# Kernel tuning notes

Measured on AMD Instinct MI355X. Metric: run time of the kernel, lower is better.

Reference implementation:

```python
import jax, jax.numpy as jnp
import numpy as np

B, L, H, D = 1, 2048, 24, 128
HID = H * D            # 3072
MLP = 4 * HID          # 12288
EPS = 1e-6


def setup_inputs() -> dict:
    key = jax.random.key(0)
    ks = jax.random.split(key, 8)
    w = lambda k, shape: jax.random.normal(k, shape, jnp.float32) * 0.02
    return {
        "x": jax.random.normal(ks[0], (B, L, HID), jnp.float32),
        "vec": jax.random.normal(ks[1], (B, HID), jnp.float32),
        "pe": jax.random.normal(ks[2], (1, 1, L, D // 2, 2, 2), jnp.float32),
        # Modulation(double=False): Dense(3*hidden)
        "mod_w": w(ks[3], (HID, 3 * HID)),
        "mod_b": jnp.zeros((3 * HID,), jnp.float32),
        # pre_norm LayerNormalization (gamma/beta)
        "ln_gamma": jnp.ones((HID,), jnp.float32),
        "ln_beta": jnp.zeros((HID,), jnp.float32),
        # linear1: Dense(3*hidden + mlp_hidden)
        "w1": w(ks[4], (HID, 3 * HID + MLP)),
        "b1": jnp.zeros((3 * HID + MLP,), jnp.float32),
        # QKNorm scales (per head_dim)
        "q_scale": jnp.ones((D,), jnp.float32),
        "k_scale": jnp.ones((D,), jnp.float32),
        # linear2: Dense(hidden), input hidden + mlp_hidden
        "w2": w(ks[5], (HID + MLP, HID)),
        "b2": jnp.zeros((HID,), jnp.float32),
    }


def _rmsnorm(t, scale):
    # RMSNorm over last (head) dim, eps=1e-6
    return t * jax.lax.rsqrt(jnp.mean(jnp.square(t), axis=-1, keepdims=True) + EPS) * scale


def _apply_rope(t, pe):
    # t: (B,H,L,D) -> view (B,H,L,D/2,1,2); pe: (1,1,L,D/2,2,2)
    t_ = t.reshape(*t.shape[:-1], -1, 1, 2)
    out = pe[..., 0] * t_[..., 0] + pe[..., 1] * t_[..., 1]  # (B,H,L,D/2,2)
    return out.reshape(t.shape)


def reference(x, vec, pe, mod_w, mod_b, ln_gamma, ln_beta, w1, b1,
              q_scale, k_scale, w2, b2):
    # Modulation: silu -> Dense -> split into shift/scale/gate, each [B,1,HID]
    mod = (jax.nn.silu(vec) @ mod_w + mod_b)[:, None, :]
    shift, scale, gate = jnp.split(mod, 3, axis=-1)

    # pre_norm LayerNorm (eps=1e-6) + modulation affine
    mu = jnp.mean(x, axis=-1, keepdims=True)
    var = jnp.mean(jnp.square(x - mu), axis=-1, keepdims=True)
    ln = (x - mu) * jax.lax.rsqrt(var + EPS) * ln_gamma + ln_beta
    x_mod = (1.0 + scale) * ln + shift

    # linear1 -> split qkv / mlp branches
    h = x_mod @ w1 + b1
    qkv, mlp = h[..., : 3 * HID], h[..., 3 * HID:]

    # 'B L (K H D) -> K B H L D'
    qkv = qkv.reshape(B, L, 3, H, D).transpose(2, 0, 3, 1, 4)
    q, k, v = qkv[0], qkv[1], qkv[2]

    # QK RMSNorm + RoPE
    q = _apply_rope(_rmsnorm(q, q_scale), pe)
    k = _apply_rope(_rmsnorm(k, k_scale), pe)

    # scaled dot-product attention
    scores = jnp.einsum("bhqd,bhkd->bhqk", q, k) * (D ** -0.5)
    attn = jnp.einsum("bhqk,bhkd->bhqd", jax.nn.softmax(scores, axis=-1), v)
    attn = attn.transpose(0, 2, 1, 3).reshape(B, L, HID)  # B H L D -> B L (H D)

    # concat attention + gelu(mlp, tanh approx) -> linear2, gated residual
    out = jnp.concatenate([attn, jax.nn.gelu(mlp, approximate=True)], axis=-1) @ w2 + b2
    return x + gate * out
```

## Files before the change

### kernel.cpp

```cpp
#include <hip/hip_runtime.h>
#include <hip/hip_bf16.h>
#include <cstdint>

#define L_SEQ 2048
#define NH    24
#define DH    128
#define HID   3072
#define MLPD  12288
#define N1    21504
#define K2    15360
#define EPSF  1e-6f
#define ATT_SCALE 0.08838834764831845f

typedef __bf16 bf16x8 __attribute__((ext_vector_type(8)));
typedef float  f32x4  __attribute__((ext_vector_type(4)));

__device__ __forceinline__ float gelu_tanh(float x) {
    float x3 = x * x * x;
    return 0.5f * x * (1.f + tanhf(0.7978845608028654f * (x + 0.044715f * x3)));
}

__device__ __forceinline__ unsigned short f2bf(float f) {
    union { float f; unsigned int u; } x{f};
    unsigned int r = x.u + 0x7fffu + ((x.u >> 16) & 1u);
    return (unsigned short)(r >> 16);
}

__device__ __forceinline__ void gload_lds16(const void* g, void* l) {
    __builtin_amdgcn_global_load_lds(
        (__attribute__((address_space(1))) void*)g,
        (__attribute__((address_space(3))) void*)l, 16, 0, 0);
}

__global__ __launch_bounds__(256)
void k_convT(const float* __restrict__ in, unsigned short* __restrict__ out,
             int R, int C) {
    __shared__ unsigned short s[64][72];
    const int r0 = blockIdx.y * 64, c0 = blockIdx.x * 64;
    const int tid = threadIdx.x;
    const int row = tid >> 4, c4 = (tid & 15) * 4;
    #pragma unroll
    for (int rr = 0; rr < 4; rr++) {
        int r = row + rr * 16;
        float4 v = *(const float4*)&in[(size_t)(r0 + r) * C + c0 + c4];
        s[r][c4 + 0] = f2bf(v.x); s[r][c4 + 1] = f2bf(v.y);
        s[r][c4 + 2] = f2bf(v.z); s[r][c4 + 3] = f2bf(v.w);
    }
    __syncthreads();
    #pragma unroll
    for (int rr = 0; rr < 4; rr++) {
        int oc = row + rr * 16;
        ushort4 t = make_ushort4(s[c4 + 0][oc], s[c4 + 1][oc],
                                 s[c4 + 2][oc], s[c4 + 3][oc]);
        *(ushort4*)&out[(size_t)(c0 + oc) * R + r0 + c4] = t;
    }
}

__global__ __launch_bounds__(256)
void k_mod(const float* __restrict__ vec, const float* __restrict__ mod_w,
           const float* __restrict__ mod_b, float* __restrict__ mod) {
    __shared__ float sv[384];
    const int j  = blockIdx.x * 256 + threadIdx.x;
    const int k0 = blockIdx.y * 384;
    for (int i = threadIdx.x; i < 384; i += 256) {
        float v = vec[k0 + i];
        sv[i] = v / (1.f + __expf(-v));
    }
    __syncthreads();
    float acc = (blockIdx.y == 0) ? mod_b[j] : 0.f;
    #pragma unroll 8
    for (int i = 0; i < 384; i++)
        acc = fmaf(sv[i], mod_w[(size_t)(k0 + i) * 9216 + j], acc);
    atomicAdd(&mod[j], acc);
}

__global__ __launch_bounds__(256)
void k_ln(const float* __restrict__ x, const float* __restrict__ mod,
          const float* __restrict__ gamma, const float* __restrict__ beta,
          unsigned short* __restrict__ x_mod) {
    __shared__ float rs_[4], rs2_[4];
    const int l = blockIdx.x, tid = threadIdx.x;
    const float* xr = x + (size_t)l * HID;
    float s = 0.f, s2 = 0.f;
    for (int i = tid; i < HID; i += 256) {
        float v = xr[i]; s += v; s2 = fmaf(v, v, s2);
    }
    #pragma unroll
    for (int off = 32; off; off >>= 1) { s += __shfl_xor(s, off); s2 += __shfl_xor(s2, off); }
    const int w = tid >> 6;
    if ((tid & 63) == 0) { rs_[w] = s; rs2_[w] = s2; }
    __syncthreads();
    s  = rs_[0] + rs_[1] + rs_[2] + rs_[3];
    s2 = rs2_[0] + rs2_[1] + rs2_[2] + rs2_[3];
    float mu   = s * (1.f / HID);
    float var  = s2 * (1.f / HID) - mu * mu;
    float rstd = rsqrtf(var + EPSF);
    unsigned short* orow = x_mod + (size_t)l * HID;
    for (int i = tid; i < HID; i += 256) {
        float ln = (xr[i] - mu) * rstd * gamma[i] + beta[i];
        orow[i] = f2bf(fmaf(1.f + mod[HID + i], ln, mod[i]));
    }
}

template<int MODE>
__global__ __launch_bounds__(256)
void gemm_bt(const unsigned short* __restrict__ A,
             const unsigned short* __restrict__ Bt,
             const float* __restrict__ bias, int K,
             float* __restrict__ qkv, unsigned short* __restrict__ vt,
             unsigned short* __restrict__ a2,
             const float* __restrict__ xres, const float* __restrict__ mod,
             float* __restrict__ out) {
    __shared__ unsigned short As[128 * 32];
    __shared__ unsigned short Bs[128 * 32];
    const int tid = threadIdx.x;
    const int bm = blockIdx.y * 128, bn = blockIdx.x * 128;
    const int w = tid >> 6, lane = tid & 63;
    const int wm = w >> 1, wn = w & 1;
    const int quad = lane >> 4, lr = lane & 15;
    const int srow = lane >> 2, spart = lane & 3;

    f32x4 acc[4][4] = {};

    for (int k0 = 0; k0 < K; k0 += 32) {
        #pragma unroll
        for (int s = 0; s < 2; s++) {
            const int slot = w + s * 4;
            gload_lds16(&A [(size_t)(bm + slot * 16 + srow) * K + k0 + spart * 8],
                        &As[slot * 512]);
            gload_lds16(&Bt[(size_t)(bn + slot * 16 + srow) * K + k0 + spart * 8],
                        &Bs[slot * 512]);
        }
        __syncthreads();
        bf16x8 af[4], bfr[4];
        #pragma unroll
        for (int t = 0; t < 4; t++) {
            af[t]  = *(const bf16x8*)&As[(wm * 64 + t * 16 + lr) * 32 + quad * 8];
            bfr[t] = *(const bf16x8*)&Bs[(wn * 64 + t * 16 + lr) * 32 + quad * 8];
        }
        #pragma unroll
        for (int mt = 0; mt < 4; mt++)
            #pragma unroll
            for (int nt = 0; nt < 4; nt++)
                acc[mt][nt] = __builtin_amdgcn_mfma_f32_16x16x32_bf16(
                    af[mt], bfr[nt], acc[mt][nt], 0, 0, 0);
        __syncthreads();
    }

    #pragma unroll
    for (int mt = 0; mt < 4; mt++) {
        #pragma unroll
        for (int nt = 0; nt < 4; nt++) {
            const int col = bn + wn * 64 + nt * 16 + lr;
            const float bs = bias[col];
            #pragma unroll
            for (int r = 0; r < 4; r++) {
                const int row = bm + wm * 64 + mt * 16 + quad * 4 + r;
                float v = acc[mt][nt][r] + bs;
                if (MODE == 0) {
                    if (col < 2 * HID) {
                        int s3 = col / HID, rem = col - s3 * HID;
                        int hh = rem >> 7, d = rem & 127;
                        qkv[(((size_t)s3 * NH + hh) * L_SEQ + row) * DH + d] = v;
                    } else if (col < 3 * HID) {
                        int rem = col - 2 * HID;
                        int hh = rem >> 7, d = rem & 127;
                        vt[((size_t)hh * DH + d) * L_SEQ + row] = f2bf(v);
                    } else {
                        a2[(size_t)row * K2 + col - 6144] = f2bf(gelu_tanh(v));
                    }
                } else {
                    out[(size_t)row * HID + col] =
                        fmaf(mod[2 * HID + col], v, xres[(size_t)row * HID + col]);
                }
            }
        }
    }
}

__global__ __launch_bounds__(64)
void k_rmsrope(const float* __restrict__ qkv, const float* __restrict__ pe,
               const float* __restrict__ qsc, const float* __restrict__ ksc,
               unsigned short* __restrict__ qb, unsigned short* __restrict__ kb) {
    const int idx = blockIdx.x;
    const int h = idx >> 11, l = idx & 2047;
    const int p = threadIdx.x;
    const float* qp = qkv + ((size_t)h * L_SEQ + l) * DH;
    const float* kp = qkv + ((size_t)(NH + h) * L_SEQ + l) * DH;
    const float4 pv = *(const float4*)&pe[((size_t)l * 64 + p) * 4];
    const float2 qs2 = *(const float2*)&qsc[2 * p];
    const float2 ks2 = *(const float2*)&ksc[2 * p];

    float2 t = *(const float2*)&qp[2 * p];
    float ss = fmaf(t.x, t.x, t.y * t.y);
    #pragma unroll
    for (int off = 32; off; off >>= 1) ss += __shfl_xor(ss, off);
    float r = rsqrtf(ss * (1.f / DH) + EPSF);
    float a = t.x * r * qs2.x, b = t.y * r * qs2.y;
    *(ushort2*)&qb[((size_t)h * L_SEQ + l) * DH + 2 * p] =
        make_ushort2(f2bf(fmaf(pv.x, a, pv.y * b) * ATT_SCALE),
                     f2bf(fmaf(pv.z, a, pv.w * b) * ATT_SCALE));

    t = *(const float2*)&kp[2 * p];
    ss = fmaf(t.x, t.x, t.y * t.y);
    #pragma unroll
    for (int off = 32; off; off >>= 1) ss += __shfl_xor(ss, off);
    r = rsqrtf(ss * (1.f / DH) + EPSF);
    a = t.x * r * ks2.x; b = t.y * r * ks2.y;
    *(ushort2*)&kb[((size_t)h * L_SEQ + l) * DH + 2 * p] =
        make_ushort2(f2bf(fmaf(pv.x, a, pv.y * b)), f2bf(fmaf(pv.z, a, pv.w * b)));
}

__global__ __launch_bounds__(256)
void attn_mfma(const unsigned short* __restrict__ qb,
               const unsigned short* __restrict__ kb,
               const unsigned short* __restrict__ vt,
               unsigned short* __restrict__ a2) {
    __shared__ unsigned short Ks[64 * 128];
    __shared__ unsigned short Vts[128 * 64];
    __shared__ unsigned short Ps[4][16][72];
    const int h = blockIdx.y;
    const int q0 = blockIdx.x * 64;
    const int tid = threadIdx.x;
    const int w = tid >> 6, lane = tid & 63;
    const int quad = lane >> 4, lr = lane & 15;
    const unsigned short* Qp = qb + (size_t)h * L_SEQ * DH;
    const unsigned short* Kp = kb + (size_t)h * L_SEQ * DH;
    const unsigned short* Vp = vt + (size_t)h * DH * L_SEQ;

    bf16x8 qf[4];
    #pragma unroll
    for (int c = 0; c < 4; c++)
        qf[c] = *(const bf16x8*)&Qp[(size_t)(q0 + w * 16 + lr) * DH + c * 32 + quad * 8];

    f32x4 acc[8] = {};
    float m[4], lsum[4];
    #pragma unroll
    for (int r = 0; r < 4; r++) { m[r] = -1e30f; lsum[r] = 0.f; }

    for (int kt = 0; kt < L_SEQ; kt += 64) {
        __syncthreads();
        #pragma unroll
        for (int j = 0; j < 4; j++) {
            const int rb = w * 16 + j * 4;
            const int row = rb + (lane >> 4);
            const int lc = (lane & 15) ^ (row & 7);
            gload_lds16(&Kp[(size_t)(kt + row) * DH + lc * 8], &Ks[rb * 128]);
        }
        #pragma unroll
        for (int j = 0; j < 4; j++) {
            const int rb = w * 32 + j * 8;
            const int row = rb + (lane >> 3);
            const int lc = (lane & 7) ^ (row & 7);
            gload_lds16(&Vp[(size_t)row * L_SEQ + kt + lc * 8], &Vts[rb * 64]);
        }
        __syncthreads();

        f32x4 s[4] = {};
        #pragma unroll
        for (int c = 0; c < 4; c++) {
            #pragma unroll
            for (int n = 0; n < 4; n++) {
                const int row = n * 16 + lr;
                const bf16x8 kf = *(const bf16x8*)
                    &Ks[row * 128 + (((c * 4 + quad) ^ (row & 7)) * 8)];
                s[n] = __builtin_amdgcn_mfma_f32_16x16x32_bf16(qf[c], kf, s[n], 0, 0, 0);
            }
        }

        float alpha[4];
        #pragma unroll
        for (int r = 0; r < 4; r++) {
            float t = fmaxf(fmaxf(s[0][r], s[1][r]), fmaxf(s[2][r], s[3][r]));
            t = fmaxf(t, __shfl_xor(t, 1));
            t = fmaxf(t, __shfl_xor(t, 2));
            t = fmaxf(t, __shfl_xor(t, 4));
            t = fmaxf(t, __shfl_xor(t, 8));
            const float mn = fmaxf(m[r], t);
            alpha[r] = __expf(m[r] - mn);
            m[r] = mn;
        }
        float psum[4] = {0.f, 0.f, 0.f, 0.f};
        #pragma unroll
        for (int n = 0; n < 4; n++) {
            #pragma unroll
            for (int r = 0; r < 4; r++) {
                const float p = __expf(s[n][r] - m[r]);
                psum[r] += p;
                Ps[w][quad * 4 + r][n * 16 + lr] = f2bf(p);
            }
        }
        #pragma unroll
        for (int r = 0; r < 4; r++) {
            float t = psum[r];
            t += __shfl_xor(t, 1); t += __shfl_xor(t, 2);
            t += __shfl_xor(t, 4); t += __shfl_xor(t, 8);
            lsum[r] = lsum[r] * alpha[r] + t;
        }
        #pragma unroll
        for (int dt = 0; dt < 8; dt++)
            #pragma unroll
            for (int r = 0; r < 4; r++) acc[dt][r] *= alpha[r];

        #pragma unroll
        for (int jc = 0; jc < 2; jc++) {
            const bf16x8 pf = *(const bf16x8*)&Ps[w][lr][jc * 32 + quad * 8];
            #pragma unroll
            for (int dt = 0; dt < 8; dt++) {
                const int row = dt * 16 + lr;
                const bf16x8 vf = *(const bf16x8*)
                    &Vts[row * 64 + (((jc * 4 + quad) ^ (row & 7)) * 8)];
                acc[dt] = __builtin_amdgcn_mfma_f32_16x16x32_bf16(pf, vf, acc[dt], 0, 0, 0);
            }
        }
    }

    float inv[4];
    #pragma unroll
    for (int r = 0; r < 4; r++) inv[r] = 1.f / lsum[r];
    unsigned short* orow = a2 + (size_t)(q0 + w * 16) * K2 + h * DH;
    #pragma unroll
    for (int dt = 0; dt < 8; dt++)
        #pragma unroll
        for (int r = 0; r < 4; r++)
            orow[(size_t)(quad * 4 + r) * K2 + dt * 16 + lr] = f2bf(acc[dt][r] * inv[r]);
}

extern "C" void kernel_launch(void* const* d_in, const int* in_sizes, int n_in,
                              void* d_out, int out_size, void* d_ws, size_t ws_size,
                              hipStream_t stream) {
    (void)in_sizes; (void)n_in; (void)out_size; (void)ws_size;
    const float* x      = (const float*)d_in[0];
    const float* vec    = (const float*)d_in[1];
    const float* pe     = (const float*)d_in[2];
    const float* mod_w  = (const float*)d_in[3];
    const float* mod_b  = (const float*)d_in[4];
    const float* gamma  = (const float*)d_in[5];
    const float* beta   = (const float*)d_in[6];
    const float* w1     = (const float*)d_in[7];
    const float* b1     = (const float*)d_in[8];
    const float* q_s    = (const float*)d_in[9];
    const float* k_s    = (const float*)d_in[10];
    const float* w2     = (const float*)d_in[11];
    const float* b2     = (const float*)d_in[12];
    float* out = (float*)d_out;

    char* ws = (char*)d_ws;
    size_t off = 0;
    float* modbuf = (float*)(ws + off);                  off += 40960;
    unsigned short* x_mod = (unsigned short*)(ws + off); off += (size_t)L_SEQ * HID * 2;
    float* qkv = (float*)(ws + off);                     off += (size_t)2 * NH * L_SEQ * DH * 4;
    unsigned short* qb  = (unsigned short*)(ws + off);   off += (size_t)NH * L_SEQ * DH * 2;
    unsigned short* kb  = (unsigned short*)(ws + off);   off += (size_t)NH * L_SEQ * DH * 2;
    unsigned short* vtb = (unsigned short*)(ws + off);   off += (size_t)NH * L_SEQ * DH * 2;
    unsigned short* a2  = (unsigned short*)(ws + off);   off += (size_t)L_SEQ * K2 * 2;
    unsigned short* w1t = (unsigned short*)(ws + off);   off += (size_t)N1 * HID * 2;
    unsigned short* w2t = (unsigned short*)(ws + off);   off += (size_t)HID * K2 * 2;

    k_convT<<<dim3(N1 / 64, HID / 64), 256, 0, stream>>>(w1, w1t, HID, N1);
    k_convT<<<dim3(HID / 64, K2 / 64), 256, 0, stream>>>(w2, w2t, K2, HID);

    hipMemsetAsync(modbuf, 0, 9216 * sizeof(float), stream);
    k_mod<<<dim3(36, 8), 256, 0, stream>>>(vec, mod_w, mod_b, modbuf);
    k_ln<<<L_SEQ, 256, 0, stream>>>(x, modbuf, gamma, beta, x_mod);

    gemm_bt<0><<<dim3(N1 / 128, L_SEQ / 128), 256, 0, stream>>>(
        x_mod, w1t, b1, HID, qkv, vtb, a2, nullptr, nullptr, nullptr);

    k_rmsrope<<<NH * L_SEQ, 64, 0, stream>>>(qkv, pe, q_s, k_s, qb, kb);
    attn_mfma<<<dim3(L_SEQ / 64, NH), 256, 0, stream>>>(qb, kb, vtb, a2);

    gemm_bt<1><<<dim3(HID / 128, L_SEQ / 128), 256, 0, stream>>>(
        a2, w2t, b2, K2, nullptr, nullptr, nullptr, x, modbuf, out);
}
```

Baseline: 1.585 ms.

## Replace GEMMs with 256x256 double-buffered 8-wave kernel, split-K linear2, pipeline attention K loads

The 128x128 single-buffered GEMM is replaced by a 256x256 tile, 8-wave kernel. It uses 128KB of dynamic LDS with double buffering, XOR-swizzled layout, interleaved stage/compute phases, partial vmcnt waits and s_setprio around MFMA bursts. linear2 now uses split-K by 2 into fp32 partials stored in the reused qkv buffer, and a new elementwise kernel does the bias, gate and residual. Attention double-buffers K tiles, prefetching the next tile while computing, and raises wave priority during MFMAs. These aim to raise MFMA utilization and hide global-load latency, at the cost of an extra partial-sum pass and fragile hand-tuned waitcnt counts.

```diff
diff --git a/kernel.cpp b/kernel.cpp
--- a/kernel.cpp
+++ b/kernel.cpp
@@ -103,79 +103,167 @@
 }
 
 template<int MODE>
-__global__ __launch_bounds__(256)
-void gemm_bt(const unsigned short* __restrict__ A,
-             const unsigned short* __restrict__ Bt,
-             const float* __restrict__ bias, int K,
-             float* __restrict__ qkv, unsigned short* __restrict__ vt,
-             unsigned short* __restrict__ a2,
-             const float* __restrict__ xres, const float* __restrict__ mod,
-             float* __restrict__ out) {
-    __shared__ unsigned short As[128 * 32];
-    __shared__ unsigned short Bs[128 * 32];
+__global__ __launch_bounds__(512, 2)
+void gemm8(const unsigned short* __restrict__ A,
+           const unsigned short* __restrict__ Bt,
+           const float* __restrict__ bias, int K, int nkt,
+           float* __restrict__ qkv, unsigned short* __restrict__ vt,
+           unsigned short* __restrict__ a2, float* __restrict__ part) {
+    extern __shared__ unsigned short sm[];
+    unsigned short* As = sm;
+    unsigned short* Bs = sm + 32768;
     const int tid = threadIdx.x;
-    const int bm = blockIdx.y * 128, bn = blockIdx.x * 128;
     const int w = tid >> 6, lane = tid & 63;
-    const int wm = w >> 1, wn = w & 1;
+    const int wm = w >> 2, wn = w & 3;
     const int quad = lane >> 4, lr = lane & 15;
-    const int srow = lane >> 2, spart = lane & 3;
-
-    f32x4 acc[4][4] = {};
-
-    for (int k0 = 0; k0 < K; k0 += 32) {
-        #pragma unroll
-        for (int s = 0; s < 2; s++) {
-            const int slot = w + s * 4;
-            gload_lds16(&A [(size_t)(bm + slot * 16 + srow) * K + k0 + spart * 8],
-                        &As[slot * 512]);
-            gload_lds16(&Bt[(size_t)(bn + slot * 16 + srow) * K + k0 + spart * 8],
-                        &Bs[slot * 512]);
-        }
-        __syncthreads();
-        bf16x8 af[4], bfr[4];
-        #pragma unroll
-        for (int t = 0; t < 4; t++) {
-            af[t]  = *(const bf16x8*)&As[(wm * 64 + t * 16 + lr) * 32 + quad * 8];
-            bfr[t] = *(const bf16x8*)&Bs[(wn * 64 + t * 16 + lr) * 32 + quad * 8];
-        }
-        #pragma unroll
-        for (int mt = 0; mt < 4; mt++)
-            #pragma unroll
-            for (int nt = 0; nt < 4; nt++)
-                acc[mt][nt] = __builtin_amdgcn_mfma_f32_16x16x32_bf16(
-                    af[mt], bfr[nt], acc[mt][nt], 0, 0, 0);
-        __syncthreads();
-    }
-
-    #pragma unroll
-    for (int mt = 0; mt < 4; mt++) {
-        #pragma unroll
-        for (int nt = 0; nt < 4; nt++) {
-            const int col = bn + wn * 64 + nt * 16 + lr;
+    const int bm = blockIdx.y * 256, bn = blockIdx.x * 256;
+    const int koff = (MODE == 1) ? blockIdx.z * (K >> 1) : 0;
+
+    f32x4 acc[8][4] = {};
+    bf16x8 a_[4][2], b_[2][2];
+
+#define STG(SEL, HM, KT, D) do {                                             \
+    const unsigned short* gp_ = (SEL) ? Bt : A;                              \
+    const int gb_ = (SEL) ? bn : bm;                                         \
+    unsigned short* ls_ = ((SEL) ? Bs : As) + (D) * 16384 + (HM) * 8192      \
+                          + ((tid & ~63) << 3);                              \
+    _Pragma("unroll")                                                        \
+    for (int q_ = 0; q_ < 2; q_++) {                                         \
+        int idx_ = q_ * 512 + tid;                                           \
+        int r_   = (HM) * 128 + (idx_ >> 3);                                 \
+        gload_lds16(&gp_[(size_t)(gb_ + r_) * K + koff + (KT) * 64           \
+                         + (((idx_ & 7) ^ (r_ & 7)) << 3)],                  \
+                    ls_ + q_ * 4096);                                        \
+    }                                                                        \
+} while (0)
+
+#define LDA(MH, D) do {                                                      \
+    _Pragma("unroll")                                                        \
+    for (int i_ = 0; i_ < 4; i_++)                                           \
+    _Pragma("unroll")                                                        \
+    for (int ks_ = 0; ks_ < 2; ks_++) {                                      \
+        int r_ = (MH) * 128 + i_ * 32 + wm * 16 + lr;                        \
+        int c_ = ks_ * 4 + quad;                                             \
+        a_[i_][ks_] = *(const bf16x8*)&As[(D) * 16384 + r_ * 64              \
+                                          + ((c_ ^ (r_ & 7)) << 3)];         \
+    }                                                                        \
+} while (0)
+
+#define LDB(NH, D) do {                                                      \
+    _Pragma("unroll")                                                        \
+    for (int j_ = 0; j_ < 2; j_++)                                           \
+    _Pragma("unroll")                                                        \
+    for (int ks_ = 0; ks_ < 2; ks_++) {                                      \
+        int r_ = (NH) * 128 + j_ * 64 + wn * 16 + lr;                        \
+        int c_ = ks_ * 4 + quad;                                             \
+        b_[j_][ks_] = *(const bf16x8*)&Bs[(D) * 16384 + r_ * 64              \
+                                          + ((c_ ^ (r_ & 7)) << 3)];         \
+    }                                                                        \
+} while (0)
+
+#define MM(MH, NH) do {                                                      \
+    __builtin_amdgcn_s_setprio(1);                                           \
+    _Pragma("unroll")                                                        \
+    for (int i_ = 0; i_ < 4; i_++)                                           \
+    _Pragma("unroll")                                                        \
+    for (int j_ = 0; j_ < 2; j_++)                                           \
+    _Pragma("unroll")                                                        \
+    for (int ks_ = 0; ks_ < 2; ks_++)                                        \
+        acc[(MH) * 4 + i_][(NH) * 2 + j_] =                                  \
+            __builtin_amdgcn_mfma_f32_16x16x32_bf16(                         \
+                a_[i_][ks_], b_[j_][ks_],                                    \
+                acc[(MH) * 4 + i_][(NH) * 2 + j_], 0, 0, 0);                 \
+    __builtin_amdgcn_s_setprio(0);                                           \
+} while (0)
+
+#define SYNC1 do { asm volatile("s_waitcnt vmcnt(4)" ::: "memory");          \
+    __builtin_amdgcn_s_barrier(); __builtin_amdgcn_sched_barrier(0); } while (0)
+#define SYNC2 do { asm volatile("" ::: "memory");                            \
+    __builtin_amdgcn_s_barrier(); __builtin_amdgcn_sched_barrier(0); } while (0)
+
+    STG(0, 0, 0, 0); STG(1, 0, 0, 0); STG(0, 1, 0, 0); STG(1, 1, 0, 0);
+    SYNC1;
+
+    for (int kt = 0; kt < nkt; ++kt) {
+        const int d = kt & 1, dn = d ^ 1;
+        const int ktn = (kt + 1 < nkt) ? kt + 1 : 0;
+        LDA(0, d); LDB(0, d);
+        STG(0, 0, ktn, dn);
+        SYNC1; MM(0, 0); SYNC2;
+        LDA(1, d);
+        STG(1, 0, ktn, dn);
+        SYNC1; MM(1, 0); SYNC2;
+        LDB(1, d);
+        STG(0, 1, ktn, dn);
+        SYNC1; MM(1, 1); SYNC2;
+        LDA(0, d);
+        STG(1, 1, ktn, dn);
+        SYNC1; MM(0, 1); SYNC2;
+    }
+
+#undef STG
+#undef LDA
+#undef LDB
+#undef MM
+#undef SYNC1
+#undef SYNC2
+
+    float* pz = (MODE == 1) ? part + (size_t)blockIdx.z * L_SEQ * HID : nullptr;
+
+    #pragma unroll
+    for (int mh = 0; mh < 2; mh++)
+    #pragma unroll
+    for (int i = 0; i < 4; i++)
+    #pragma unroll
+    for (int nh = 0; nh < 2; nh++)
+    #pragma unroll
+    for (int j = 0; j < 2; j++) {
+        const int col  = bn + nh * 128 + j * 64 + wn * 16 + lr;
+        const int row0 = bm + mh * 128 + i * 32 + wm * 16 + quad * 4;
+        const f32x4 v4 = acc[mh * 4 + i][nh * 2 + j];
+        if (MODE == 0) {
             const float bs = bias[col];
             #pragma unroll
             for (int r = 0; r < 4; r++) {
-                const int row = bm + wm * 64 + mt * 16 + quad * 4 + r;
-                float v = acc[mt][nt][r] + bs;
-                if (MODE == 0) {
-                    if (col < 2 * HID) {
-                        int s3 = col / HID, rem = col - s3 * HID;
-                        int hh = rem >> 7, d = rem & 127;
-                        qkv[(((size_t)s3 * NH + hh) * L_SEQ + row) * DH + d] = v;
-                    } else if (col < 3 * HID) {
-                        int rem = col - 2 * HID;
-                        int hh = rem >> 7, d = rem & 127;
-                        vt[((size_t)hh * DH + d) * L_SEQ + row] = f2bf(v);
-                    } else {
-                        a2[(size_t)row * K2 + col - 6144] = f2bf(gelu_tanh(v));
-                    }
+                const int row = row0 + r;
+                float v = v4[r] + bs;
+                if (col < 2 * HID) {
+                    int s3 = col / HID, rem = col - s3 * HID;
+                    int hh = rem >> 7, dd = rem & 127;
+                    qkv[(((size_t)s3 * NH + hh) * L_SEQ + row) * DH + dd] = v;
+                } else if (col < 3 * HID) {
+                    int rem = col - 2 * HID;
+                    int hh = rem >> 7, dd = rem & 127;
+                    vt[((size_t)hh * DH + dd) * L_SEQ + row] = f2bf(v);
                 } else {
-                    out[(size_t)row * HID + col] =
-                        fmaf(mod[2 * HID + col], v, xres[(size_t)row * HID + col]);
+                    a2[(size_t)row * K2 + col - 6144] = f2bf(gelu_tanh(v));
                 }
             }
-        }
-    }
+        } else {
+            #pragma unroll
+            for (int r = 0; r < 4; r++)
+                pz[(size_t)(row0 + r) * HID + col] = v4[r];
+        }
+    }
+}
+
+__global__ __launch_bounds__(256)
+void k_fin(const float* __restrict__ p, const float* __restrict__ x,
+           const float* __restrict__ mod, const float* __restrict__ b2,
+           float* __restrict__ out) {
+    const int col = blockIdx.x * 1024 + threadIdx.x * 4;
+    const size_t i = (size_t)blockIdx.y * HID + col;
+    float4 a  = *(const float4*)&p[i];
+    float4 b  = *(const float4*)&p[(size_t)L_SEQ * HID + i];
+    float4 xr = *(const float4*)&x[i];
+    float4 g  = *(const float4*)&mod[2 * HID + col];
+    float4 bb = *(const float4*)&b2[col];
+    float4 o;
+    o.x = fmaf(g.x, a.x + b.x + bb.x, xr.x);
+    o.y = fmaf(g.y, a.y + b.y + bb.y, xr.y);
+    o.z = fmaf(g.z, a.z + b.z + bb.z, xr.z);
+    o.w = fmaf(g.w, a.w + b.w + bb.w, xr.w);
+    *(float4*)&out[i] = o;
 }
 
 __global__ __launch_bounds__(64)
@@ -216,7 +304,7 @@
                const unsigned short* __restrict__ kb,
                const unsigned short* __restrict__ vt,
                unsigned short* __restrict__ a2) {
-    __shared__ unsigned short Ks[64 * 128];
+    __shared__ unsigned short Ks[2][64 * 128];
     __shared__ unsigned short Vts[128 * 64];
     __shared__ unsigned short Ps[4][16][72];
     const int h = blockIdx.y;
@@ -233,20 +321,25 @@
     for (int c = 0; c < 4; c++)
         qf[c] = *(const bf16x8*)&Qp[(size_t)(q0 + w * 16 + lr) * DH + c * 32 + quad * 8];
 
+    #pragma unroll
+    for (int j = 0; j < 4; j++) {
+        const int rb = w * 16 + j * 4;
+        const int row = rb + (lane >> 4);
+        const int lc = (lane & 15) ^ (row & 7);
+        gload_lds16(&Kp[(size_t)row * DH + lc * 8], &Ks[0][rb * 128]);
+    }
+
     f32x4 acc[8] = {};
     float m[4], lsum[4];
     #pragma unroll
     for (int r = 0; r < 4; r++) { m[r] = -1e30f; lsum[r] = 0.f; }
 
     for (int kt = 0; kt < L_SEQ; kt += 64) {
-        __syncthreads();
-        #pragma unroll
-        for (int j = 0; j < 4; j++) {
-            const int rb = w * 16 + j * 4;
-            const int row = rb + (lane >> 4);
-            const int lc = (lane & 15) ^ (row & 7);
-            gload_lds16(&Kp[(size_t)(kt + row) * DH + lc * 8], &Ks[rb * 128]);
-        }
+        const int d = (kt >> 6) & 1;
+        const int ktn = (kt + 64 < L_SEQ) ? kt + 64 : 0;
+        asm volatile("s_waitcnt vmcnt(0)" ::: "memory");
+        __builtin_amdgcn_s_barrier();
+        __builtin_amdgcn_sched_barrier(0);
         #pragma unroll
         for (int j = 0; j < 4; j++) {
             const int rb = w * 32 + j * 8;
@@ -254,19 +347,27 @@
             const int lc = (lane & 7) ^ (row & 7);
             gload_lds16(&Vp[(size_t)row * L_SEQ + kt + lc * 8], &Vts[rb * 64]);
         }
-        __syncthreads();
+        #pragma unroll
+        for (int j = 0; j < 4; j++) {
+            const int rb = w * 16 + j * 4;
+            const int row = rb + (lane >> 4);
+            const int lc = (lane & 15) ^ (row & 7);
+            gload_lds16(&Kp[(size_t)(ktn + row) * DH + lc * 8], &Ks[d ^ 1][rb * 128]);
+        }
 
         f32x4 s[4] = {};
+        __builtin_amdgcn_s_setprio(1);
         #pragma unroll
         for (int c = 0; c < 4; c++) {
             #pragma unroll
             for (int n = 0; n < 4; n++) {
                 const int row = n * 16 + lr;
                 const bf16x8 kf = *(const bf16x8*)
-                    &Ks[row * 128 + (((c * 4 + quad) ^ (row & 7)) * 8)];
+                    &Ks[d][row * 128 + (((c * 4 + quad) ^ (row & 7)) * 8)];
                 s[n] = __builtin_amdgcn_mfma_f32_16x16x32_bf16(qf[c], kf, s[n], 0, 0, 0);
             }
         }
+        __builtin_amdgcn_s_setprio(0);
 
         float alpha[4];
         #pragma unroll
@@ -302,6 +403,11 @@
             #pragma unroll
             for (int r = 0; r < 4; r++) acc[dt][r] *= alpha[r];
 
+        asm volatile("s_waitcnt vmcnt(4)" ::: "memory");
+        __builtin_amdgcn_s_barrier();
+        __builtin_amdgcn_sched_barrier(0);
+
+        __builtin_amdgcn_s_setprio(1);
         #pragma unroll
         for (int jc = 0; jc < 2; jc++) {
             const bf16x8 pf = *(const bf16x8*)&Ps[w][lr][jc * 32 + quad * 8];
@@ -313,6 +419,7 @@
                 acc[dt] = __builtin_amdgcn_mfma_f32_16x16x32_bf16(pf, vf, acc[dt], 0, 0, 0);
             }
         }
+        __builtin_amdgcn_s_setprio(0);
     }
 
     float inv[4];
@@ -356,6 +463,16 @@
     unsigned short* a2  = (unsigned short*)(ws + off);   off += (size_t)L_SEQ * K2 * 2;
     unsigned short* w1t = (unsigned short*)(ws + off);   off += (size_t)N1 * HID * 2;
     unsigned short* w2t = (unsigned short*)(ws + off);   off += (size_t)HID * K2 * 2;
+    float* part = qkv;
+
+    static bool s_init = false;
+    if (!s_init) {
+        s_init = true;
+        hipFuncSetAttribute(reinterpret_cast<const void*>(&gemm8<0>),
+                            hipFuncAttributeMaxDynamicSharedMemorySize, 131072);
+        hipFuncSetAttribute(reinterpret_cast<const void*>(&gemm8<1>),
+                            hipFuncAttributeMaxDynamicSharedMemorySize, 131072);
+    }
 
     k_convT<<<dim3(N1 / 64, HID / 64), 256, 0, stream>>>(w1, w1t, HID, N1);
     k_convT<<<dim3(HID / 64, K2 / 64), 256, 0, stream>>>(w2, w2t, K2, HID);
@@ -364,12 +481,14 @@
     k_mod<<<dim3(36, 8), 256, 0, stream>>>(vec, mod_w, mod_b, modbuf);
     k_ln<<<L_SEQ, 256, 0, stream>>>(x, modbuf, gamma, beta, x_mod);
 
-    gemm_bt<0><<<dim3(N1 / 128, L_SEQ / 128), 256, 0, stream>>>(
-        x_mod, w1t, b1, HID, qkv, vtb, a2, nullptr, nullptr, nullptr);
+    gemm8<0><<<dim3(N1 / 256, L_SEQ / 256, 1), 512, 131072, stream>>>(
+        x_mod, w1t, b1, HID, HID / 64, qkv, vtb, a2, nullptr);
 
     k_rmsrope<<<NH * L_SEQ, 64, 0, stream>>>(qkv, pe, q_s, k_s, qb, kb);
     attn_mfma<<<dim3(L_SEQ / 64, NH), 256, 0, stream>>>(qb, kb, vtb, a2);
 
-    gemm_bt<1><<<dim3(HID / 128, L_SEQ / 128), 256, 0, stream>>>(
-        a2, w2t, b2, K2, nullptr, nullptr, nullptr, x, modbuf, out);
-}
+    gemm8<1><<<dim3(HID / 256, L_SEQ / 256, 2), 512, 131072, stream>>>(
+        a2, w2t, nullptr, K2, K2 / 2 / 64, nullptr, nullptr, nullptr, part);
+
+    k_fin<<<dim3(HID / 1024, L_SEQ), 256, 0, stream>>>(part, x, modbuf, b2, out);
+}
```

New measurement: 1.341 ms. -15.4%, faster.
